# Optimization experiments

Hardware: AMD Instinct MI355X
Metric: run time of the kernel (lower is better)

The kernel has to match this reference:

```python
import jax, jax.numpy as jnp
import numpy as np
import itertools

B, G, FIN, T = 8, 2048, 32, 10
H = 64
DIM = 2
M = 5            # kernel_size per dim
K = M ** DIM     # 25 spline weights
E = 262144
N = B * G

_BITS = np.array(list(itertools.product([0, 1], repeat=DIM)), dtype=np.int32)  # [S, DIM]
_STRIDES = (M ** np.arange(DIM)).astype(np.int32)                              # [DIM]


def _spline_basis(edge_attr):
    """Degree-1 open B-spline basis. Returns basis [E,S] (float) and widx [E,S] (int)."""
    frac = edge_attr * (M - 1)                       # pseudo in [0,1] -> [0, M-1]
    k0 = jnp.clip(jnp.floor(frac), 0, M - 2)
    t = frac - k0                                    # [E, DIM]
    k0 = k0.astype(jnp.int32)
    bits = jnp.asarray(_BITS)                        # [S, DIM]
    tb = jnp.where(bits[None] == 1, t[:, None, :], 1.0 - t[:, None, :])  # [E,S,DIM]
    basis = jnp.prod(tb, axis=-1)                    # [E, S]
    widx = jnp.sum((k0[:, None, :] + bits[None]) * jnp.asarray(_STRIDES)[None, None, :], axis=-1)
    return basis, widx                               # widx: [E, S] in [0, K)


def _spline_conv(x, W, Wroot, b, src, dst, basis, widx):
    # x: [N, Fin]; W: [K, Fin, Fout]; Wroot: [Fin, Fout]; b: [Fout]
    xw = jnp.einsum('nf,kfo->nko', x, W)             # [N, K, Fout]
    g = xw[src[:, None], widx]                       # [E, S, Fout]
    msg = jnp.einsum('es,eso->eo', basis, g)         # [E, Fout]
    agg = jax.ops.segment_sum(msg, dst, num_segments=N)
    deg = jax.ops.segment_sum(jnp.ones((src.shape[0],), x.dtype), dst, num_segments=N)
    return agg / jnp.maximum(deg, 1.0)[:, None] + x @ Wroot + b


def setup_inputs() -> dict:
    key = jax.random.key(0)
    ks = jax.random.split(key, 20)
    inp = {
        'x': jax.random.normal(ks[0], (B, G, FIN, T), dtype=jnp.float32),
        'edge_index': jax.random.randint(ks[1], (2, E), 0, N, dtype=jnp.int64),
        'edge_attr': jax.random.uniform(ks[2], (E, DIM), dtype=jnp.float32),
    }
    names = ['xr', 'hr', 'xz', 'hz', 'xn']
    for i, nm in enumerate(names):
        fin = FIN if nm[0] == 'x' else H
        k1, k2, k3 = jax.random.split(ks[3 + i], 3)
        inp[f'W_{nm}'] = jax.random.normal(k1, (K, fin, H), dtype=jnp.float32) * 0.05
        inp[f'root_{nm}'] = jax.random.normal(k2, (fin, H), dtype=jnp.float32) * 0.05
        inp[f'b_{nm}'] = jax.random.normal(k3, (H,), dtype=jnp.float32) * 0.05
    return inp


def reference(x, edge_index, edge_attr,
              W_xr, root_xr, b_xr, W_hr, root_hr, b_hr,
              W_xz, root_xz, b_xz, W_hz, root_hz, b_hz,
              W_xn, root_xn, b_xn):
    src = edge_index[0].astype(jnp.int32)
    dst = edge_index[1].astype(jnp.int32)
    basis, widx = _spline_basis(edge_attr)  # shared across all 6 conv calls

    conv = lambda v, W, Wr, b: _spline_conv(v, W, Wr, b, src, dst, basis, widx)

    def cell(h, xt):
        hr = conv(h, W_hr, root_hr, b_hr)  # computed once, used in r and n (original calls it twice)
        r = jax.nn.sigmoid(conv(xt, W_xr, root_xr, b_xr) + hr)
        z = jax.nn.sigmoid(conv(xt, W_xz, root_xz, b_xz) + conv(h, W_hz, root_hz, b_hz))
        n = jnp.tanh(conv(xt, W_xn, root_xn, b_xn) + r * hr)
        h_new = (1.0 - z) * n + z * h
        return h_new, h_new

    xs = jnp.moveaxis(x, -1, 0).reshape(T, N, FIN)   # [T, N, Fin]
    h0 = jnp.zeros((N, H), x.dtype)
    h_last, hs = jax.lax.scan(cell, h0, xs)          # hs: [T, N, H]

    layer_output = jnp.transpose(hs.reshape(T, B, G, H), (1, 2, 3, 0))  # [B, G, H, T]
    last_state = h_last.reshape(1, B, G, H)
    return layer_output, last_state
```

## Files before the change

kernel.cpp:

```cpp
#include <hip/hip_runtime.h>
#include <hip/hip_bf16.h>
#include <hip/hip_fp16.h>

#define NNODE 16384
#define EDGES 262144
#define HOUT 64
#define TSTEPS 10
#define KT_H 1664
#define KT_X 832
#define NB 16
#define NBX 16

typedef __attribute__((ext_vector_type(8))) short bf16x8;
typedef __attribute__((ext_vector_type(4))) float f32x4;
typedef unsigned short u16;

__device__ __forceinline__ u16 f2b(float x) {
  __hip_bfloat16 b = __float2bfloat16(x);
  return *reinterpret_cast<const u16*>(&b);
}
__device__ __forceinline__ float b2f(u16 v) {
  union { unsigned u; float f; } c;
  c.u = ((unsigned)v) << 16;
  return c.f;
}


__global__ __launch_bounds__(256) void xpose_kernel(const float* __restrict__ x,
                                                    u16* __restrict__ xTb) {
  const int i = blockIdx.x * 256 + threadIdx.x;
  if (i >= NNODE * 32) return;
  const float* src = x + (size_t)i * TSTEPS;
  #pragma unroll
  for (int t = 0; t < TSTEPS; ++t)
    xTb[(size_t)t * NNODE * 32 + i] = f2b(src[t]);
}

__device__ __forceinline__ int cell_of(float a0, float a1, float4* b) {
  const float f0 = a0 * 4.f, f1 = a1 * 4.f;
  const float k0f = fminf(fmaxf(floorf(f0), 0.f), 3.f);
  const float k1f = fminf(fmaxf(floorf(f1), 0.f), 3.f);
  const float t0 = f0 - k0f, t1 = f1 - k1f;
  b->x = (1.f - t0) * (1.f - t1);
  b->y = (1.f - t0) * t1;
  b->z = t0 * (1.f - t1);
  b->w = t0 * t1;
  return (int)k0f + 4 * (int)k1f;
}

__global__ __launch_bounds__(256) void cellcount_kernel(const int* __restrict__ ei,
                                                        const float* __restrict__ ea,
                                                        int* __restrict__ cnt) {
  const int e = blockIdx.x * 256 + threadIdx.x;
  if (e >= EDGES) return;
  const int d = ei[EDGES + e];
  float4 b;
  const int cell = cell_of(ea[2 * e], ea[2 * e + 1], &b);
  atomicAdd(&cnt[d * 16 + cell], 1);
}

__global__ __launch_bounds__(256) void nodesum_kernel(const int* __restrict__ cnt,
                                                      int* __restrict__ degi) {
  const int d = blockIdx.x * 256 + threadIdx.x;
  if (d >= NNODE) return;
  int s = 0;
  #pragma unroll
  for (int c = 0; c < 16; ++c) s += cnt[d * 16 + c];
  degi[d] = s;
}

__global__ __launch_bounds__(1024) void scan_kernel(const int* __restrict__ degi,
                                                    int* __restrict__ rp,
                                                    float* __restrict__ deg_inv) {
  __shared__ int sh[1024];
  const int tid = threadIdx.x;
  const int base = tid * 16;
  int loc[16];
  int sum = 0;
  #pragma unroll
  for (int i = 0; i < 16; ++i) { loc[i] = degi[base + i]; sum += loc[i]; }
  sh[tid] = sum;
  __syncthreads();
  for (int off = 1; off < 1024; off <<= 1) {
    int v = 0;
    if (tid >= off) v = sh[tid - off];
    __syncthreads();
    if (tid >= off) sh[tid] += v;
    __syncthreads();
  }
  int ex = sh[tid] - sum;
  #pragma unroll
  for (int i = 0; i < 16; ++i) {
    rp[base + i] = ex;
    ex += loc[i];
    deg_inv[base + i] = 1.f / (float)max(loc[i], 1);
  }
  if (tid == 1023) rp[NNODE] = ex;
}

__global__ __launch_bounds__(256) void rp2_kernel(const int* __restrict__ rp,
                                                  const int* __restrict__ cnt,
                                                  int* __restrict__ rp2) {
  const int d = blockIdx.x * 256 + threadIdx.x;
  if (d >= NNODE) return;
  int base = rp[d];
  #pragma unroll
  for (int c = 0; c < 16; ++c) {
    rp2[d * 16 + c] = base;
    base += cnt[d * 16 + c];
  }
  if (d == NNODE - 1) rp2[NNODE * 16] = base;
}

__global__ __launch_bounds__(256) void scatter2_kernel(const int* __restrict__ ei,
                                                       const float* __restrict__ ea,
                                                       const int* __restrict__ rp2,
                                                       int* __restrict__ cursor2,
                                                       int* __restrict__ esrc,
                                                       float4* __restrict__ ebasis) {
  const int e = blockIdx.x * 256 + threadIdx.x;
  if (e >= EDGES) return;
  const int s = ei[e];
  const int d = ei[EDGES + e];
  float4 b;
  const int cell = cell_of(ea[2 * e], ea[2 * e + 1], &b);
  const int pos = rp2[d * 16 + cell] + atomicAdd(&cursor2[d * 16 + cell], 1);
  esrc[pos] = s;
  ebasis[pos] = b;
}

__global__ __launch_bounds__(256) void wprep_kernel(const float* __restrict__ W,
                                                    const float* __restrict__ root,
                                                    u16* __restrict__ out,
                                                    int kspfin, int kt) {
  const int i = blockIdx.x * 256 + threadIdx.x;
  if (i >= 64 * kt) return;
  const int o = i / kt, kf = i % kt;
  const float v = (kf < kspfin) ? W[(size_t)kf * 64 + o]
                                : root[(size_t)(kf - kspfin) * 64 + o];
  out[(size_t)o * kt + kf] = f2b(v);
}

#define SEC(K0, K1, BND)                                               \
  {                                                                    \
    const int eC = (BND);                                              \
    for (; e < eC; ++e) {                                              \
      const int sD = p.esrc[e + 3];                                    \
      const float4 b2 = p.ebasis[e + 2];                               \
      const float v2 = GATHER(sC);                                     \
      acc[(K0) + 5 * (K1)]     += b0.x * v0;                           \
      acc[(K0) + 5 * (K1) + 1] += b0.z * v0;                           \
      acc[(K0) + 5 * (K1) + 5] += b0.y * v0;                           \
      acc[(K0) + 5 * (K1) + 6] += b0.w * v0;                           \
      b0 = b1; b1 = b2; v0 = v1; v1 = v2; sC = sD;                     \
    }                                                                  \
  }

#define SEC_ALL                                                        \
  SEC(0, 0, q0.y) SEC(1, 0, q0.z) SEC(2, 0, q0.w) SEC(3, 0, q1.x)     \
  SEC(0, 1, q1.y) SEC(1, 1, q1.z) SEC(2, 1, q1.w) SEC(3, 1, q2.x)     \
  SEC(0, 2, q2.y) SEC(1, 2, q2.z) SEC(2, 2, q2.w) SEC(3, 2, q3.x)     \
  SEC(0, 3, q3.y) SEC(1, 3, q3.z) SEC(2, 3, q3.w) SEC(3, 3, eEnd)


struct XP {
  const u16* xTb;
  const int* rp2;
  const int* esrc;
  const float4* ebasis;
  const float* deg_inv;
  const u16* WxrT; const u16* WxzT; const u16* WxnT;
  const float* b_xr; const float* b_xz; const float* b_xn;
  __half* xcr; __half* xcz; __half* xcn;
};

__global__ __launch_bounds__(256, 4) void xc_kernel(XP p) {
  __shared__ __align__(16) u16 UXb[2 * NBX * KT_X];
  const int tid = threadIdx.x;
  const int wave = tid >> 6, lane = tid & 63;
  const int half = lane >> 5, fl = lane & 31;
  const int tp = blockIdx.y * 2;
  const int d0 = blockIdx.x * NBX;
  const u16* __restrict__ xb = p.xTb + (size_t)(tp + half) * NNODE * 32;

  #pragma unroll 1
  for (int nn = 0; nn < 4; ++nn) {
    const int dloc = wave * 4 + nn;
    const int d = d0 + dloc;
    float acc[25];
    #pragma unroll
    for (int k = 0; k < 25; ++k) acc[k] = 0.f;
    const int4 q0 = *(const int4*)(p.rp2 + d * 16);
    const int4 q1 = *(const int4*)(p.rp2 + d * 16 + 4);
    const int4 q2 = *(const int4*)(p.rp2 + d * 16 + 8);
    const int4 q3 = *(const int4*)(p.rp2 + d * 16 + 12);
    const int eEnd = p.rp2[d * 16 + 16];
    int e = q0.x;
    #define GATHER(S) b2f(xb[((S) << 5) + fl])
    int sC;
    float4 b0, b1;
    float v0, v1;
    {
      const int sA = p.esrc[e], sB = p.esrc[e + 1];
      sC = p.esrc[e + 2];
      b0 = p.ebasis[e]; b1 = p.ebasis[e + 1];
      v0 = GATHER(sA); v1 = GATHER(sB);
    }
    SEC_ALL
    #undef GATHER
    const float di = p.deg_inv[d];
    const int row = dloc + half * 16;
    u16* ux = UXb + row * KT_X;
    const int sw = (row & 7) << 3;
    #pragma unroll
    for (int k = 0; k < 25; ++k) ux[(k * 32 + fl) ^ sw] = f2b(acc[k] * di);
    ux[(800 + fl) ^ sw] = xb[(d << 5) + fl];
  }
  __syncthreads();

  const int col = lane & 15, q = lane >> 4;
  const int o = wave * 16 + col;
  const int swc = (col & 7) << 3;
  f32x4 a0r, a0z, a0n, a1r, a1z, a1n;
  { const float b = p.b_xr[o]; a0r = f32x4{b, b, b, b}; a1r = a0r; }
  { const float b = p.b_xz[o]; a0z = f32x4{b, b, b, b}; a1z = a0z; }
  { const float b = p.b_xn[o]; a0n = f32x4{b, b, b, b}; a1n = a0n; }
  const u16* bXr = p.WxrT + (size_t)o * KT_X + 8 * q;
  const u16* bXz = p.WxzT + (size_t)o * KT_X + 8 * q;
  const u16* bXn = p.WxnT + (size_t)o * KT_X + 8 * q;
  #pragma unroll 2
  for (int ks = 0; ks < KT_X / 32; ++ks) {
    const int ofs = (ks * 32 + q * 8) ^ swc;
    const bf16x8 a0 = *reinterpret_cast<const bf16x8*>(UXb + col * KT_X + ofs);
    const bf16x8 a1 = *reinterpret_cast<const bf16x8*>(UXb + (col + 16) * KT_X + ofs);
    const bf16x8 wr = *reinterpret_cast<const bf16x8*>(bXr + ks * 32);
    const bf16x8 wz = *reinterpret_cast<const bf16x8*>(bXz + ks * 32);
    const bf16x8 wn = *reinterpret_cast<const bf16x8*>(bXn + ks * 32);
    a0r = __builtin_amdgcn_mfma_f32_16x16x32_bf16(a0, wr, a0r, 0, 0, 0);
    a0z = __builtin_amdgcn_mfma_f32_16x16x32_bf16(a0, wz, a0z, 0, 0, 0);
    a0n = __builtin_amdgcn_mfma_f32_16x16x32_bf16(a0, wn, a0n, 0, 0, 0);
    a1r = __builtin_amdgcn_mfma_f32_16x16x32_bf16(a1, wr, a1r, 0, 0, 0);
    a1z = __builtin_amdgcn_mfma_f32_16x16x32_bf16(a1, wz, a1z, 0, 0, 0);
    a1n = __builtin_amdgcn_mfma_f32_16x16x32_bf16(a1, wn, a1n, 0, 0, 0);
  }

  #pragma unroll
  for (int j = 0; j < 4; ++j) {
    const int node = d0 + q * 4 + j;
    const size_t i0 = (size_t)tp * NNODE * 64 + (size_t)node * 64 + o;
    const size_t i1 = i0 + (size_t)NNODE * 64;
    p.xcr[i0] = __float2half(a0r[j]);
    p.xcz[i0] = __float2half(a0z[j]);
    p.xcn[i0] = __float2half(a0n[j]);
    p.xcr[i1] = __float2half(a1r[j]);
    p.xcz[i1] = __float2half(a1z[j]);
    p.xcn[i1] = __float2half(a1n[j]);
  }
}


struct GP {
  const float* h_cur;
  const u16* h_curb;
  float* h_next;
  u16* h_nextb;
  const int* rp2;
  const int* esrc;
  const float4* ebasis;
  const float* deg_inv;
  const u16* WhrT; const u16* WhzT;
  const float* b_hr; const float* b_hz;
  const __half* xcr; const __half* xcz; const __half* xcn;
  u16* hs;
};

__global__ __launch_bounds__(512, 4) void gcgru_step(GP p, int t) {
  __shared__ __align__(16) u16 UHb[NB * KT_H];
  __shared__ float gates[2][NB][HOUT];
  const int tid = threadIdx.x;
  const int wave = tid >> 6, lane = tid & 63;
  const int d0 = blockIdx.x * NB;

  #pragma unroll 1
  for (int nn = 0; nn < 2; ++nn) {
    const int dloc = wave * 2 + nn;
    const int d = d0 + dloc;
    float acc[25];
    #pragma unroll
    for (int k = 0; k < 25; ++k) acc[k] = 0.f;
    const int4 q0 = *(const int4*)(p.rp2 + d * 16);
    const int4 q1 = *(const int4*)(p.rp2 + d * 16 + 4);
    const int4 q2 = *(const int4*)(p.rp2 + d * 16 + 8);
    const int4 q3 = *(const int4*)(p.rp2 + d * 16 + 12);
    const int eEnd = p.rp2[d * 16 + 16];
    int e = q0.x;
    #define GATHER(S) b2f(p.h_curb[((S) << 6) + lane])
    int sC;
    float4 b0, b1;
    float v0, v1;
    {
      const int sA = p.esrc[e], sB = p.esrc[e + 1];
      sC = p.esrc[e + 2];
      b0 = p.ebasis[e]; b1 = p.ebasis[e + 1];
      v0 = GATHER(sA); v1 = GATHER(sB);
    }
    SEC_ALL
    #undef GATHER
    const float di = p.deg_inv[d];
    u16* uh = UHb + dloc * KT_H;
    const int sw = (dloc & 7) << 3;
    #pragma unroll
    for (int k = 0; k < 25; ++k) uh[(k * 64 + lane) ^ sw] = f2b(acc[k] * di);
    uh[(1600 + lane) ^ sw] = p.h_curb[(d << 6) + lane];
  }
  __syncthreads();

  const int col = lane & 15, q = lane >> 4;
  const int conv = wave & 1, ot = wave >> 1;
  const int o = ot * 16 + col;
  const int swc = (col & 7) << 3;
  const u16* WT = conv ? p.WhzT : p.WhrT;
  const float bias = conv ? p.b_hz[o] : p.b_hr[o];
  f32x4 a = f32x4{bias, bias, bias, bias};
  const u16* bW = WT + (size_t)o * KT_H + 8 * q;
  #pragma unroll 4
  for (int ks = 0; ks < KT_H / 32; ++ks) {
    const bf16x8 af =
        *reinterpret_cast<const bf16x8*>(UHb + col * KT_H + ((ks * 32 + q * 8) ^ swc));
    const bf16x8 wf = *reinterpret_cast<const bf16x8*>(bW + ks * 32);
    a = __builtin_amdgcn_mfma_f32_16x16x32_bf16(af, wf, a, 0, 0, 0);
  }
  #pragma unroll
  for (int j = 0; j < 4; ++j) gates[conv][q * 4 + j][o] = a[j];
  __syncthreads();

  #pragma unroll
  for (int rep = 0; rep < 2; ++rep) {
    const int i = tid + rep * 512;
    const int nloc = i >> 6, oo = i & 63;
    const int node = d0 + nloc;
    const size_t idx = (size_t)node * 64 + oo;
    const size_t tix = (size_t)t * NNODE * 64 + idx;
    const float hrv = gates[0][nloc][oo];
    const float hzv = gates[1][nloc][oo];
    const float xrv = __half2float(p.xcr[tix]);
    const float xzv = __half2float(p.xcz[tix]);
    const float xnv = __half2float(p.xcn[tix]);
    const float r = 1.f / (1.f + __expf(-(xrv + hrv)));
    const float z = 1.f / (1.f + __expf(-(xzv + hzv)));
    const float ng = 1.f - 2.f / (__expf(2.f * (xnv + r * hrv)) + 1.f);
    const float hp = p.h_cur[idx];
    const float hn = (1.f - z) * ng + z * hp;
    p.h_next[idx] = hn;
    const u16 hb = f2b(hn);
    p.h_nextb[idx] = hb;
    p.hs[tix] = hb;
  }
}


__global__ __launch_bounds__(256) void finalize_kernel(const u16* __restrict__ hs,
                                                       float* __restrict__ out,
                                                       float* __restrict__ out_last) {
  const int i = blockIdx.x * 256 + threadIdx.x;
  if (i >= NNODE * 64) return;
  float* ob = out + (size_t)(i >> 6) * 640 + (size_t)(i & 63) * 10;
  #pragma unroll
  for (int t = 0; t < TSTEPS; ++t)
    ob[t] = b2f(hs[(size_t)t * NNODE * 64 + i]);
  out_last[i] = b2f(hs[(size_t)9 * NNODE * 64 + i]);
}


extern "C" void kernel_launch(void* const* d_in, const int* in_sizes, int n_in,
                              void* d_out, int out_size, void* d_ws, size_t ws_size,
                              hipStream_t stream) {
  const float* x = (const float*)d_in[0];
  const int* ei = (const int*)d_in[1];
  const float* ea = (const float*)d_in[2];
  const float* W_xr = (const float*)d_in[3];
  const float* root_xr = (const float*)d_in[4];
  const float* b_xr = (const float*)d_in[5];
  const float* W_hr = (const float*)d_in[6];
  const float* root_hr = (const float*)d_in[7];
  const float* b_hr = (const float*)d_in[8];
  const float* W_xz = (const float*)d_in[9];
  const float* root_xz = (const float*)d_in[10];
  const float* b_xz = (const float*)d_in[11];
  const float* W_hz = (const float*)d_in[12];
  const float* root_hz = (const float*)d_in[13];
  const float* b_hz = (const float*)d_in[14];
  const float* W_xn = (const float*)d_in[15];
  const float* root_xn = (const float*)d_in[16];
  const float* b_xn = (const float*)d_in[17];

  char* w = (char*)d_ws;
  u16* xTb = (u16*)w;          w += (size_t)TSTEPS * NNODE * 32 * 2;
  __half* xcr = (__half*)w;    w += (size_t)TSTEPS * NNODE * 64 * 2;
  __half* xcz = (__half*)w;    w += (size_t)TSTEPS * NNODE * 64 * 2;
  __half* xcn = (__half*)w;    w += (size_t)TSTEPS * NNODE * 64 * 2;
  u16* hs = (u16*)w;           w += (size_t)TSTEPS * NNODE * 64 * 2;
  float* h0 = (float*)w;       w += (size_t)NNODE * HOUT * 4;
  float* h1 = (float*)w;       w += (size_t)NNODE * HOUT * 4;
  u16* h0b = (u16*)w;          w += (size_t)NNODE * HOUT * 2;
  u16* h1b = (u16*)w;          w += (size_t)NNODE * HOUT * 2;
  float4* ebasis = (float4*)w; w += (size_t)(EDGES + 16) * 16;
  int* esrc = (int*)w;         w += (size_t)(EDGES + 16) * 4;
  u16* WhrT = (u16*)w;         w += (size_t)64 * KT_H * 2;
  u16* WhzT = (u16*)w;         w += (size_t)64 * KT_H * 2;
  u16* WxrT = (u16*)w;         w += (size_t)64 * KT_X * 2;
  u16* WxzT = (u16*)w;         w += (size_t)64 * KT_X * 2;
  u16* WxnT = (u16*)w;         w += (size_t)64 * KT_X * 2;
  int* cnt = (int*)w;          w += (size_t)NNODE * 16 * 4;
  int* cursor2 = (int*)w;      w += (size_t)NNODE * 16 * 4;
  int* rp2 = (int*)w;          w += (size_t)(NNODE * 16 + 16) * 4;
  int* degi = (int*)w;         w += (size_t)NNODE * 4;
  int* rp = (int*)w;           w += (size_t)(NNODE + 4) * 4;
  float* deg_inv = (float*)w;  w += (size_t)NNODE * 4;

  hipMemsetAsync(cnt, 0, (size_t)NNODE * 16 * 4, stream);
  hipMemsetAsync(cursor2, 0, (size_t)NNODE * 16 * 4, stream);
  hipMemsetAsync(h0, 0, (size_t)NNODE * HOUT * 4, stream);
  hipMemsetAsync(h0b, 0, (size_t)NNODE * HOUT * 2, stream);
  hipMemsetAsync((void*)(ebasis + EDGES), 0, 16 * 16, stream);
  hipMemsetAsync(esrc + EDGES, 0, 16 * 4, stream);

  xpose_kernel<<<(NNODE * 32 + 255) / 256, 256, 0, stream>>>(x, xTb);
  cellcount_kernel<<<(EDGES + 255) / 256, 256, 0, stream>>>(ei, ea, cnt);
  nodesum_kernel<<<(NNODE + 255) / 256, 256, 0, stream>>>(cnt, degi);
  scan_kernel<<<1, 1024, 0, stream>>>(degi, rp, deg_inv);
  rp2_kernel<<<(NNODE + 255) / 256, 256, 0, stream>>>(rp, cnt, rp2);
  scatter2_kernel<<<(EDGES + 255) / 256, 256, 0, stream>>>(ei, ea, rp2, cursor2,
                                                           esrc, ebasis);
  wprep_kernel<<<(64 * KT_H + 255) / 256, 256, 0, stream>>>(W_hr, root_hr, WhrT, 1600, KT_H);
  wprep_kernel<<<(64 * KT_H + 255) / 256, 256, 0, stream>>>(W_hz, root_hz, WhzT, 1600, KT_H);
  wprep_kernel<<<(64 * KT_X + 255) / 256, 256, 0, stream>>>(W_xr, root_xr, WxrT, 800, KT_X);
  wprep_kernel<<<(64 * KT_X + 255) / 256, 256, 0, stream>>>(W_xz, root_xz, WxzT, 800, KT_X);
  wprep_kernel<<<(64 * KT_X + 255) / 256, 256, 0, stream>>>(W_xn, root_xn, WxnT, 800, KT_X);

  XP xp;
  xp.xTb = xTb;
  xp.rp2 = rp2;
  xp.esrc = esrc;
  xp.ebasis = ebasis;
  xp.deg_inv = deg_inv;
  xp.WxrT = WxrT; xp.WxzT = WxzT; xp.WxnT = WxnT;
  xp.b_xr = b_xr; xp.b_xz = b_xz; xp.b_xn = b_xn;
  xp.xcr = xcr; xp.xcz = xcz; xp.xcn = xcn;
  xc_kernel<<<dim3(NNODE / NBX, TSTEPS / 2), 256, 0, stream>>>(xp);

  GP p;
  p.rp2 = rp2;
  p.esrc = esrc;
  p.ebasis = ebasis;
  p.deg_inv = deg_inv;
  p.WhrT = WhrT; p.WhzT = WhzT;
  p.b_hr = b_hr; p.b_hz = b_hz;
  p.xcr = xcr; p.xcz = xcz; p.xcn = xcn;
  p.hs = hs;

  float* ha = h0; float* hb_ = h1;
  u16* hab = h0b; u16* hbb = h1b;
  for (int t = 0; t < TSTEPS; ++t) {
    p.h_cur = ha; p.h_curb = hab;
    p.h_next = hb_; p.h_nextb = hbb;
    gcgru_step<<<NNODE / NB, 512, 0, stream>>>(p, t);
    float* tf = ha; ha = hb_; hb_ = tf;
    u16* tb = hab; hab = hbb; hbb = tb;
  }

  float* out = (float*)d_out;
  float* out_last = out + (size_t)NNODE * HOUT * TSTEPS;
  finalize_kernel<<<(NNODE * 64 + 255) / 256, 256, 0, stream>>>(hs, out, out_last);
}
```

Baseline: 1.487 ms.

## Split fused edge-gather+GEMM kernels into separate passes with MFMA-fragment layouts

Each fused kernel is split in two. An edge aggregation kernel (one wave per node) writes the aggregated features to global memory, already arranged in MFMA operand fragment order. A separate GEMM kernel then loads these fragments directly and uses weights pre-packed in fragment order by a new wprep kernel. The aim is to decouple the irregular gather from the MFMA work and remove the LDS swizzling and shared-memory staging in the x path. The cost is a round trip through global memory for the intermediate U matrices and twice as many kernel launches per timestep.

```diff
diff --git a/kernel.cpp b/kernel.cpp
--- a/kernel.cpp
+++ b/kernel.cpp
@@ -6,10 +6,8 @@
 #define EDGES 262144
 #define HOUT 64
 #define TSTEPS 10
-#define KT_H 1664
-#define KT_X 832
-#define NB 16
-#define NBX 16
+#define NKT_H 52
+#define NKT_X 26
 
 typedef __attribute__((ext_vector_type(8))) short bf16x8;
 typedef __attribute__((ext_vector_type(4))) float f32x4;
@@ -129,16 +127,19 @@
   ebasis[pos] = b;
 }
 
-__global__ __launch_bounds__(256) void wprep_kernel(const float* __restrict__ W,
-                                                    const float* __restrict__ root,
-                                                    u16* __restrict__ out,
-                                                    int kspfin, int kt) {
+__global__ __launch_bounds__(256) void wprep_frag(const float* __restrict__ W,
+                                                  const float* __restrict__ root,
+                                                  u16* __restrict__ out,
+                                                  int kspfin, int nkt) {
+  const int K = nkt * 32;
   const int i = blockIdx.x * 256 + threadIdx.x;
-  if (i >= 64 * kt) return;
-  const int o = i / kt, kf = i % kt;
-  const float v = (kf < kspfin) ? W[(size_t)kf * 64 + o]
-                                : root[(size_t)(kf - kspfin) * 64 + o];
-  out[(size_t)o * kt + kf] = f2b(v);
+  if (i >= 64 * K) return;
+  const int o = i / K, k = i % K;
+  const float v = (k < kspfin) ? W[(size_t)k * 64 + o]
+                               : root[(size_t)(k - kspfin) * 64 + o];
+  const int ot = o >> 4, kt = k >> 5;
+  const int lif = (o & 15) + (((k & 31) >> 3) << 4);
+  out[(((size_t)(ot * nkt + kt)) << 9) + lif * 8 + (k & 7)] = f2b(v);
 }
 
 #define SEC(K0, K1, BND)                                               \
@@ -162,187 +163,179 @@
   SEC(0, 2, q2.y) SEC(1, 2, q2.z) SEC(2, 2, q2.w) SEC(3, 2, q3.x)     \
   SEC(0, 3, q3.y) SEC(1, 3, q3.z) SEC(2, 3, q3.w) SEC(3, 3, eEnd)
 
-
-struct XP {
+#define SEC_PROLOGUE                                                   \
+  const int4 q0 = *(const int4*)(p.rp2 + d * 16);                      \
+  const int4 q1 = *(const int4*)(p.rp2 + d * 16 + 4);                  \
+  const int4 q2 = *(const int4*)(p.rp2 + d * 16 + 8);                  \
+  const int4 q3 = *(const int4*)(p.rp2 + d * 16 + 12);                 \
+  const int eEnd = p.rp2[d * 16 + 16];                                 \
+  int e = q0.x;                                                        \
+  int sC;                                                              \
+  float4 b0, b1;                                                       \
+  float v0, v1;                                                        \
+  {                                                                    \
+    const int sA = p.esrc[e], sB = p.esrc[e + 1];                      \
+    sC = p.esrc[e + 2];                                                \
+    b0 = p.ebasis[e]; b1 = p.ebasis[e + 1];                            \
+    v0 = GATHER(sA); v1 = GATHER(sB);                                  \
+  }
+
+
+struct HEP {
+  const u16* h_curb;
+  const int* rp2;
+  const int* esrc;
+  const float4* ebasis;
+  const float* deg_inv;
+  u16* Uh;
+};
+
+__global__ __launch_bounds__(256) void edge_h(HEP p) {
+  const int wave = threadIdx.x >> 6, lane = threadIdx.x & 63;
+  const int d = blockIdx.x * 4 + wave;
+  float acc[25];
+  #pragma unroll
+  for (int k = 0; k < 25; ++k) acc[k] = 0.f;
+  #define GATHER(S) b2f(p.h_curb[((S) << 6) + lane])
+  SEC_PROLOGUE
+  SEC_ALL
+  #undef GATHER
+  const float di = p.deg_inv[d];
+  const int rt = d >> 4;
+  const int lif8 = ((d & 15) + (((lane & 31) >> 3) << 4)) * 8 + (lane & 7);
+  u16* ug = p.Uh + (((size_t)rt * NKT_H) << 9) + lif8;
+  const int kth = lane >> 5;
+  #pragma unroll
+  for (int c = 0; c < 25; ++c)
+    ug[(size_t)(2 * c + kth) << 9] = f2b(acc[c] * di);
+  ug[(size_t)(50 + kth) << 9] = p.h_curb[(d << 6) + lane];
+}
+
+struct XEP {
   const u16* xTb;
   const int* rp2;
   const int* esrc;
   const float4* ebasis;
   const float* deg_inv;
-  const u16* WxrT; const u16* WxzT; const u16* WxnT;
+  u16* Ux;
+};
+
+__global__ __launch_bounds__(256) void edge_x(XEP p, int tp) {
+  const int wave = threadIdx.x >> 6, lane = threadIdx.x & 63;
+  const int half = lane >> 5, fl = lane & 31;
+  const int d = blockIdx.x * 4 + wave;
+  const u16* __restrict__ xb = p.xTb + (size_t)(tp * 2 + half) * NNODE * 32;
+  float acc[25];
+  #pragma unroll
+  for (int k = 0; k < 25; ++k) acc[k] = 0.f;
+  #define GATHER(S) b2f(xb[((S) << 5) + fl])
+  SEC_PROLOGUE
+  SEC_ALL
+  #undef GATHER
+  const float di = p.deg_inv[d];
+  const int rt = (half << 10) + (d >> 4);
+  const int lif8 = ((d & 15) + ((fl >> 3) << 4)) * 8 + (fl & 7);
+  u16* ug = p.Ux + (((size_t)rt * NKT_X) << 9) + lif8;
+  #pragma unroll
+  for (int c = 0; c < 25; ++c)
+    ug[(size_t)c << 9] = f2b(acc[c] * di);
+  ug[(size_t)25 << 9] = xb[(d << 5) + fl];
+}
+
+
+struct XGP {
+  const u16* Ux;
+  const u16* Wxfrag;
   const float* b_xr; const float* b_xz; const float* b_xn;
   __half* xcr; __half* xcz; __half* xcn;
 };
 
-__global__ __launch_bounds__(256, 4) void xc_kernel(XP p) {
-  __shared__ __align__(16) u16 UXb[2 * NBX * KT_X];
+__global__ __launch_bounds__(768) void gemm_x(XGP p, int tp) {
   const int tid = threadIdx.x;
   const int wave = tid >> 6, lane = tid & 63;
-  const int half = lane >> 5, fl = lane & 31;
-  const int tp = blockIdx.y * 2;
-  const int d0 = blockIdx.x * NBX;
-  const u16* __restrict__ xb = p.xTb + (size_t)(tp + half) * NNODE * 32;
-
-  #pragma unroll 1
-  for (int nn = 0; nn < 4; ++nn) {
-    const int dloc = wave * 4 + nn;
-    const int d = d0 + dloc;
-    float acc[25];
+  const int g = wave >> 2, ot = wave & 3;
+  const int col = lane & 15, q = lane >> 4;
+  const int o = ot * 16 + col;
+  const float* bp = (g == 0) ? p.b_xr : (g == 1) ? p.b_xz : p.b_xn;
+  __half* outp = (g == 0) ? p.xcr : (g == 1) ? p.xcz : p.xcn;
+  const float bias = bp[o];
+  bf16x8 w[NKT_X];
+  const u16* wf = p.Wxfrag + (((size_t)(g * 4 + ot) * NKT_X) << 9) + lane * 8;
+  #pragma unroll
+  for (int kt = 0; kt < NKT_X; ++kt)
+    w[kt] = *reinterpret_cast<const bf16x8*>(wf + ((size_t)kt << 9));
+
+  for (int rl = 0; rl < 8; ++rl) {
+    const int rt = blockIdx.x * 8 + rl;
+    const u16* ua = p.Ux + (((size_t)rt * NKT_X) << 9) + lane * 8;
+    f32x4 acc = f32x4{bias, bias, bias, bias};
     #pragma unroll
-    for (int k = 0; k < 25; ++k) acc[k] = 0.f;
-    const int4 q0 = *(const int4*)(p.rp2 + d * 16);
-    const int4 q1 = *(const int4*)(p.rp2 + d * 16 + 4);
-    const int4 q2 = *(const int4*)(p.rp2 + d * 16 + 8);
-    const int4 q3 = *(const int4*)(p.rp2 + d * 16 + 12);
-    const int eEnd = p.rp2[d * 16 + 16];
-    int e = q0.x;
-    #define GATHER(S) b2f(xb[((S) << 5) + fl])
-    int sC;
-    float4 b0, b1;
-    float v0, v1;
-    {
-      const int sA = p.esrc[e], sB = p.esrc[e + 1];
-      sC = p.esrc[e + 2];
-      b0 = p.ebasis[e]; b1 = p.ebasis[e + 1];
-      v0 = GATHER(sA); v1 = GATHER(sB);
+    for (int kt = 0; kt < NKT_X; ++kt) {
+      const bf16x8 a = *reinterpret_cast<const bf16x8*>(ua + ((size_t)kt << 9));
+      acc = __builtin_amdgcn_mfma_f32_16x16x32_bf16(a, w[kt], acc, 0, 0, 0);
     }
-    SEC_ALL
-    #undef GATHER
-    const float di = p.deg_inv[d];
-    const int row = dloc + half * 16;
-    u16* ux = UXb + row * KT_X;
-    const int sw = (row & 7) << 3;
+    const int t = tp * 2 + (rt >> 10);
+    const int nbase = (rt & 1023) << 4;
     #pragma unroll
-    for (int k = 0; k < 25; ++k) ux[(k * 32 + fl) ^ sw] = f2b(acc[k] * di);
-    ux[(800 + fl) ^ sw] = xb[(d << 5) + fl];
-  }
-  __syncthreads();
-
-  const int col = lane & 15, q = lane >> 4;
-  const int o = wave * 16 + col;
-  const int swc = (col & 7) << 3;
-  f32x4 a0r, a0z, a0n, a1r, a1z, a1n;
-  { const float b = p.b_xr[o]; a0r = f32x4{b, b, b, b}; a1r = a0r; }
-  { const float b = p.b_xz[o]; a0z = f32x4{b, b, b, b}; a1z = a0z; }
-  { const float b = p.b_xn[o]; a0n = f32x4{b, b, b, b}; a1n = a0n; }
-  const u16* bXr = p.WxrT + (size_t)o * KT_X + 8 * q;
-  const u16* bXz = p.WxzT + (size_t)o * KT_X + 8 * q;
-  const u16* bXn = p.WxnT + (size_t)o * KT_X + 8 * q;
-  #pragma unroll 2
-  for (int ks = 0; ks < KT_X / 32; ++ks) {
-    const int ofs = (ks * 32 + q * 8) ^ swc;
-    const bf16x8 a0 = *reinterpret_cast<const bf16x8*>(UXb + col * KT_X + ofs);
-    const bf16x8 a1 = *reinterpret_cast<const bf16x8*>(UXb + (col + 16) * KT_X + ofs);
-    const bf16x8 wr = *reinterpret_cast<const bf16x8*>(bXr + ks * 32);
-    const bf16x8 wz = *reinterpret_cast<const bf16x8*>(bXz + ks * 32);
-    const bf16x8 wn = *reinterpret_cast<const bf16x8*>(bXn + ks * 32);
-    a0r = __builtin_amdgcn_mfma_f32_16x16x32_bf16(a0, wr, a0r, 0, 0, 0);
-    a0z = __builtin_amdgcn_mfma_f32_16x16x32_bf16(a0, wz, a0z, 0, 0, 0);
-    a0n = __builtin_amdgcn_mfma_f32_16x16x32_bf16(a0, wn, a0n, 0, 0, 0);
-    a1r = __builtin_amdgcn_mfma_f32_16x16x32_bf16(a1, wr, a1r, 0, 0, 0);
-    a1z = __builtin_amdgcn_mfma_f32_16x16x32_bf16(a1, wz, a1z, 0, 0, 0);
-    a1n = __builtin_amdgcn_mfma_f32_16x16x32_bf16(a1, wn, a1n, 0, 0, 0);
-  }
-
-  #pragma unroll
-  for (int j = 0; j < 4; ++j) {
-    const int node = d0 + q * 4 + j;
-    const size_t i0 = (size_t)tp * NNODE * 64 + (size_t)node * 64 + o;
-    const size_t i1 = i0 + (size_t)NNODE * 64;
-    p.xcr[i0] = __float2half(a0r[j]);
-    p.xcz[i0] = __float2half(a0z[j]);
-    p.xcn[i0] = __float2half(a0n[j]);
-    p.xcr[i1] = __float2half(a1r[j]);
-    p.xcz[i1] = __float2half(a1z[j]);
-    p.xcn[i1] = __float2half(a1n[j]);
-  }
-}
-
-
-struct GP {
+    for (int j = 0; j < 4; ++j) {
+      const int n = nbase + q * 4 + j;
+      outp[((size_t)t * NNODE + n) * 64 + o] = __float2half(acc[j]);
+    }
+  }
+}
+
+
+struct HGP {
+  const u16* Uh;
+  const u16* Whfrag;
+  const float* b_hr; const float* b_hz;
   const float* h_cur;
-  const u16* h_curb;
   float* h_next;
   u16* h_nextb;
-  const int* rp2;
-  const int* esrc;
-  const float4* ebasis;
-  const float* deg_inv;
-  const u16* WhrT; const u16* WhzT;
-  const float* b_hr; const float* b_hz;
   const __half* xcr; const __half* xcz; const __half* xcn;
   u16* hs;
 };
 
-__global__ __launch_bounds__(512, 4) void gcgru_step(GP p, int t) {
-  __shared__ __align__(16) u16 UHb[NB * KT_H];
-  __shared__ float gates[2][NB][HOUT];
+__global__ __launch_bounds__(512) void gemm_h(HGP p, int t) {
+  __shared__ __align__(16) float4 UA4[3328];
   const int tid = threadIdx.x;
   const int wave = tid >> 6, lane = tid & 63;
-  const int d0 = blockIdx.x * NB;
-
-  #pragma unroll 1
-  for (int nn = 0; nn < 2; ++nn) {
-    const int dloc = wave * 2 + nn;
-    const int d = d0 + dloc;
-    float acc[25];
-    #pragma unroll
-    for (int k = 0; k < 25; ++k) acc[k] = 0.f;
-    const int4 q0 = *(const int4*)(p.rp2 + d * 16);
-    const int4 q1 = *(const int4*)(p.rp2 + d * 16 + 4);
-    const int4 q2 = *(const int4*)(p.rp2 + d * 16 + 8);
-    const int4 q3 = *(const int4*)(p.rp2 + d * 16 + 12);
-    const int eEnd = p.rp2[d * 16 + 16];
-    int e = q0.x;
-    #define GATHER(S) b2f(p.h_curb[((S) << 6) + lane])
-    int sC;
-    float4 b0, b1;
-    float v0, v1;
-    {
-      const int sA = p.esrc[e], sB = p.esrc[e + 1];
-      sC = p.esrc[e + 2];
-      b0 = p.ebasis[e]; b1 = p.ebasis[e + 1];
-      v0 = GATHER(sA); v1 = GATHER(sB);
-    }
-    SEC_ALL
-    #undef GATHER
-    const float di = p.deg_inv[d];
-    u16* uh = UHb + dloc * KT_H;
-    const int sw = (dloc & 7) << 3;
-    #pragma unroll
-    for (int k = 0; k < 25; ++k) uh[(k * 64 + lane) ^ sw] = f2b(acc[k] * di);
-    uh[(1600 + lane) ^ sw] = p.h_curb[(d << 6) + lane];
+  const int rt = blockIdx.x;
+  {
+    const float4* src = (const float4*)(p.Uh + (((size_t)rt * NKT_H) << 9));
+    for (int i = tid; i < 3328; i += 512) UA4[i] = src[i];
   }
   __syncthreads();
 
+  const int g = wave & 1, ot = wave >> 1;
   const int col = lane & 15, q = lane >> 4;
-  const int conv = wave & 1, ot = wave >> 1;
   const int o = ot * 16 + col;
-  const int swc = (col & 7) << 3;
-  const u16* WT = conv ? p.WhzT : p.WhrT;
-  const float bias = conv ? p.b_hz[o] : p.b_hr[o];
-  f32x4 a = f32x4{bias, bias, bias, bias};
-  const u16* bW = WT + (size_t)o * KT_H + 8 * q;
+  const float bias = g ? p.b_hz[o] : p.b_hr[o];
+  f32x4 acc = f32x4{bias, bias, bias, bias};
+  const u16* ua = (const u16*)UA4 + lane * 8;
+  const u16* wf = p.Whfrag + (((size_t)(g * 4 + ot) * NKT_H) << 9) + lane * 8;
   #pragma unroll 4
-  for (int ks = 0; ks < KT_H / 32; ++ks) {
-    const bf16x8 af =
-        *reinterpret_cast<const bf16x8*>(UHb + col * KT_H + ((ks * 32 + q * 8) ^ swc));
-    const bf16x8 wf = *reinterpret_cast<const bf16x8*>(bW + ks * 32);
-    a = __builtin_amdgcn_mfma_f32_16x16x32_bf16(af, wf, a, 0, 0, 0);
-  }
-  #pragma unroll
-  for (int j = 0; j < 4; ++j) gates[conv][q * 4 + j][o] = a[j];
+  for (int kt = 0; kt < NKT_H; ++kt) {
+    const bf16x8 a = *reinterpret_cast<const bf16x8*>(ua + ((size_t)kt << 9));
+    const bf16x8 w = *reinterpret_cast<const bf16x8*>(wf + ((size_t)kt << 9));
+    acc = __builtin_amdgcn_mfma_f32_16x16x32_bf16(a, w, acc, 0, 0, 0);
+  }
+  __syncthreads();
+  float* gates = (float*)UA4;
+  #pragma unroll
+  for (int j = 0; j < 4; ++j)
+    gates[(g << 10) + (q * 4 + j) * 64 + o] = acc[j];
   __syncthreads();
 
   #pragma unroll
   for (int rep = 0; rep < 2; ++rep) {
     const int i = tid + rep * 512;
     const int nloc = i >> 6, oo = i & 63;
-    const int node = d0 + nloc;
+    const int node = (rt << 4) + nloc;
     const size_t idx = (size_t)node * 64 + oo;
     const size_t tix = (size_t)t * NNODE * 64 + idx;
-    const float hrv = gates[0][nloc][oo];
-    const float hzv = gates[1][nloc][oo];
+    const float hrv = gates[nloc * 64 + oo];
+    const float hzv = gates[1024 + nloc * 64 + oo];
     const float xrv = __half2float(p.xcr[tix]);
     const float xzv = __half2float(p.xcz[tix]);
     const float xnv = __half2float(p.xcn[tix]);
@@ -406,11 +399,10 @@
   u16* h1b = (u16*)w;          w += (size_t)NNODE * HOUT * 2;
   float4* ebasis = (float4*)w; w += (size_t)(EDGES + 16) * 16;
   int* esrc = (int*)w;         w += (size_t)(EDGES + 16) * 4;
-  u16* WhrT = (u16*)w;         w += (size_t)64 * KT_H * 2;
-  u16* WhzT = (u16*)w;         w += (size_t)64 * KT_H * 2;
-  u16* WxrT = (u16*)w;         w += (size_t)64 * KT_X * 2;
-  u16* WxzT = (u16*)w;         w += (size_t)64 * KT_X * 2;
-  u16* WxnT = (u16*)w;         w += (size_t)64 * KT_X * 2;
+  u16* Whfrag = (u16*)w;       w += (size_t)2 * 4 * NKT_H * 512 * 2;
+  u16* Wxfrag = (u16*)w;       w += (size_t)3 * 4 * NKT_X * 512 * 2;
+  u16* Uh = (u16*)w;           w += (size_t)1024 * NKT_H * 512 * 2;
+  u16* Ux = (u16*)w;           w += (size_t)2048 * NKT_X * 512 * 2;
   int* cnt = (int*)w;          w += (size_t)NNODE * 16 * 4;
   int* cursor2 = (int*)w;      w += (size_t)NNODE * 16 * 4;
   int* rp2 = (int*)w;          w += (size_t)(NNODE * 16 + 16) * 4;
@@ -432,39 +424,42 @@
   rp2_kernel<<<(NNODE + 255) / 256, 256, 0, stream>>>(rp, cnt, rp2);
   scatter2_kernel<<<(EDGES + 255) / 256, 256, 0, stream>>>(ei, ea, rp2, cursor2,
                                                            esrc, ebasis);
-  wprep_kernel<<<(64 * KT_H + 255) / 256, 256, 0, stream>>>(W_hr, root_hr, WhrT, 1600, KT_H);
-  wprep_kernel<<<(64 * KT_H + 255) / 256, 256, 0, stream>>>(W_hz, root_hz, WhzT, 1600, KT_H);
-  wprep_kernel<<<(64 * KT_X + 255) / 256, 256, 0, stream>>>(W_xr, root_xr, WxrT, 800, KT_X);
-  wprep_kernel<<<(64 * KT_X + 255) / 256, 256, 0, stream>>>(W_xz, root_xz, WxzT, 800, KT_X);
-  wprep_kernel<<<(64 * KT_X + 255) / 256, 256, 0, stream>>>(W_xn, root_xn, WxnT, 800, KT_X);
-
-  XP xp;
-  xp.xTb = xTb;
-  xp.rp2 = rp2;
-  xp.esrc = esrc;
-  xp.ebasis = ebasis;
-  xp.deg_inv = deg_inv;
-  xp.WxrT = WxrT; xp.WxzT = WxzT; xp.WxnT = WxnT;
-  xp.b_xr = b_xr; xp.b_xz = b_xz; xp.b_xn = b_xn;
-  xp.xcr = xcr; xp.xcz = xcz; xp.xcn = xcn;
-  xc_kernel<<<dim3(NNODE / NBX, TSTEPS / 2), 256, 0, stream>>>(xp);
-
-  GP p;
-  p.rp2 = rp2;
-  p.esrc = esrc;
-  p.ebasis = ebasis;
-  p.deg_inv = deg_inv;
-  p.WhrT = WhrT; p.WhzT = WhzT;
-  p.b_hr = b_hr; p.b_hz = b_hz;
-  p.xcr = xcr; p.xcz = xcz; p.xcn = xcn;
-  p.hs = hs;
+  const int gWH = (64 * NKT_H * 32 + 255) / 256;
+  const int gWX = (64 * NKT_X * 32 + 255) / 256;
+  wprep_frag<<<gWH, 256, 0, stream>>>(W_hr, root_hr, Whfrag, 1600, NKT_H);
+  wprep_frag<<<gWH, 256, 0, stream>>>(W_hz, root_hz, Whfrag + (size_t)4 * NKT_H * 512, 1600, NKT_H);
+  wprep_frag<<<gWX, 256, 0, stream>>>(W_xr, root_xr, Wxfrag, 800, NKT_X);
+  wprep_frag<<<gWX, 256, 0, stream>>>(W_xz, root_xz, Wxfrag + (size_t)4 * NKT_X * 512, 800, NKT_X);
+  wprep_frag<<<gWX, 256, 0, stream>>>(W_xn, root_xn, Wxfrag + (size_t)8 * NKT_X * 512, 800, NKT_X);
+
+  XEP xe;
+  xe.xTb = xTb; xe.rp2 = rp2; xe.esrc = esrc; xe.ebasis = ebasis;
+  xe.deg_inv = deg_inv; xe.Ux = Ux;
+  XGP xg;
+  xg.Ux = Ux; xg.Wxfrag = Wxfrag;
+  xg.b_xr = b_xr; xg.b_xz = b_xz; xg.b_xn = b_xn;
+  xg.xcr = xcr; xg.xcz = xcz; xg.xcn = xcn;
+  for (int tp = 0; tp < TSTEPS / 2; ++tp) {
+    edge_x<<<NNODE / 4, 256, 0, stream>>>(xe, tp);
+    gemm_x<<<256, 768, 0, stream>>>(xg, tp);
+  }
+
+  HEP he;
+  he.rp2 = rp2; he.esrc = esrc; he.ebasis = ebasis;
+  he.deg_inv = deg_inv; he.Uh = Uh;
+  HGP hg;
+  hg.Uh = Uh; hg.Whfrag = Whfrag;
+  hg.b_hr = b_hr; hg.b_hz = b_hz;
+  hg.xcr = xcr; hg.xcz = xcz; hg.xcn = xcn;
+  hg.hs = hs;
 
   float* ha = h0; float* hb_ = h1;
   u16* hab = h0b; u16* hbb = h1b;
   for (int t = 0; t < TSTEPS; ++t) {
-    p.h_cur = ha; p.h_curb = hab;
-    p.h_next = hb_; p.h_nextb = hbb;
-    gcgru_step<<<NNODE / NB, 512, 0, stream>>>(p, t);
+    he.h_curb = hab;
+    edge_h<<<NNODE / 4, 256, 0, stream>>>(he);
+    hg.h_cur = ha; hg.h_next = hb_; hg.h_nextb = hbb;
+    gemm_h<<<NNODE / 16, 512, 0, stream>>>(hg, t);
     float* tf = ha; ha = hb_; hb_ = tf;
     u16* tb = hab; hab = hbb; hbb = tb;
   }
```

Result: faster. 1.298 ms (-12.7%).
